# Kernel tuning notes

Measured on AMD Instinct MI355X. Metric: run time of the kernel, lower is better.

## Reference

```python
import jax, jax.numpy as jnp
import numpy as np

B, D_SENS, D_IDX, D_INT, D_OUT = 512, 784, 64, 32, 10
M = 262144  # eidetic memory entries


def setup_inputs() -> dict:
    key = jax.random.key(0)
    ks = jax.random.split(key, 12)
    s = lambda fan_in: 1.0 / np.sqrt(fan_in)
    return {
        "x_sensory": jax.random.normal(ks[0], (B, D_SENS), jnp.float32),
        "W1": jax.random.uniform(ks[1], (D_IDX, D_SENS), jnp.float32, -s(D_SENS), s(D_SENS)),
        "b1": jax.random.uniform(ks[2], (D_IDX,), jnp.float32, -s(D_SENS), s(D_SENS)),
        "W2": jax.random.uniform(ks[3], (D_INT, D_IDX), jnp.float32, -s(D_IDX), s(D_IDX)),
        "b2": jax.random.uniform(ks[4], (D_INT,), jnp.float32, -s(D_IDX), s(D_IDX)),
        "W3": jax.random.uniform(ks[5], (D_INT, D_SENS), jnp.float32, -s(D_SENS), s(D_SENS)),
        "b3": jax.random.uniform(ks[6], (D_INT,), jnp.float32, -s(D_SENS), s(D_SENS)),
        "W4": jax.random.uniform(ks[7], (D_OUT, D_INT), jnp.float32, -s(D_INT), s(D_INT)),
        "b4": jax.random.uniform(ks[8], (D_OUT,), jnp.float32, -s(D_INT), s(D_INT)),
        "mem_keys": jax.random.normal(ks[9], (M, D_IDX), jnp.float32),
        "mem_values": jax.random.normal(ks[10], (M, D_SENS), jnp.float32),
    }


def reference(x_sensory, W1, b1, W2, b2, W3, b3, W4, b4, mem_keys, mem_values):
    # indexer activations [B, 64]
    a_idx = jax.nn.relu(x_sensory @ W1.T + b1)
    # eidetic memory: nearest-neighbor lookup over stored indexer keys
    # squared L2 distances [B, M] via expansion (query norm is constant per row, omitted)
    d = jnp.sum(mem_keys * mem_keys, axis=1)[None, :] - 2.0 * (a_idx @ mem_keys.T)
    nn_idx = jnp.argmin(d, axis=1)  # [B]
    x_recaller = mem_values[nn_idx]  # [B, 784] irregular gather
    # integrator
    a_int = jax.nn.relu(a_idx @ W2.T + b2 + x_recaller @ W3.T + b3)
    return a_int @ W4.T + b4
```

## Files before the change

### kernel.cpp

```cpp
#include <hip/hip_runtime.h>
#include <stdint.h>

#define B_SZ   512
#define D_SENS 784
#define D_IDX  64
#define D_INT  32
#define D_OUT  10
#define M_ENT  262144
#define NCHUNK (M_ENT / 64)
#define MARGIN 1.5f

typedef __attribute__((ext_vector_type(8))) short bf16x8;
typedef __attribute__((ext_vector_type(4))) float f32x4;

__device__ inline unsigned short f2bf_rne(float f) {
    unsigned int u = __float_as_uint(f);
    unsigned int r = u + 0x7fffu + ((u >> 16) & 1u);
    return (unsigned short)(r >> 16);
}
__device__ inline unsigned int pack2bf_t(float lo, float hi) {
    return (__float_as_uint(lo) >> 16) | (__float_as_uint(hi) & 0xFFFF0000u);
}

__global__ __launch_bounds__(256) void k_front(const float* __restrict__ x,
                                               const float* __restrict__ W1,
                                               const float* __restrict__ b1,
                                               float* __restrict__ a_out,
                                               unsigned short* __restrict__ a_bf,
                                               unsigned long long* __restrict__ best) {
    int b = blockIdx.x, tid = threadIdx.x;
    __shared__ float xs[D_SENS];
    if (tid < 196) ((float4*)xs)[tid] = ((const float4*)(x + (size_t)b * D_SENS))[tid];
    if (tid == 0) best[b] = ~0ULL;
    __syncthreads();
    int i = tid >> 2, sub = tid & 3;
    const float4* wr = (const float4*)(W1 + (size_t)i * D_SENS);
    const float4* xs4 = (const float4*)xs;
    float a0 = 0.f, a1 = 0.f, a2 = 0.f, a3 = 0.f;
    #pragma unroll 7
    for (int jj = 0; jj < 49; ++jj) {
        float4 w = wr[sub + 4 * jj];
        float4 xv = xs4[sub + 4 * jj];
        a0 += w.x * xv.x; a1 += w.y * xv.y; a2 += w.z * xv.z; a3 += w.w * xv.w;
    }
    float s = (a0 + a1) + (a2 + a3);
    s += __shfl_xor(s, 1, 64);
    s += __shfl_xor(s, 2, 64);
    if (sub == 0) {
        float v = s + b1[i];
        float r = v > 0.f ? v : 0.f;
        a_out[b * D_IDX + i] = r;
        a_bf[b * D_IDX + i] = f2bf_rne(r);
    }
}

__global__ __launch_bounds__(256) void k_screen(const float* __restrict__ keys,
                                                const unsigned short* __restrict__ ab,
                                                float* __restrict__ chunkmin) {
    __shared__ unsigned short qlds[B_SZ * D_IDX];
    __shared__ float cms[8][B_SZ];
    int tid = threadIdx.x;
    int lane = tid & 63, wid = tid >> 6;
    int l15 = lane & 15, lg = lane >> 4;

    {
        int r = tid >> 3, j = tid & 7;
        #pragma unroll
        for (int pass = 0; pass < 16; ++pass, r += 32) {
            uint4 v = *(const uint4*)((const char*)ab + r * 128 + j * 16);
            int boff = r * 128 + ((j * 16) ^ ((r & 7) << 4));
            *(uint4*)((char*)qlds + boff) = v;
        }
    }

    int mbase = blockIdx.x * 512 + wid * 128;
    bf16x8 kf[8][2];
    f32x4 nrmv[8];
    #pragma unroll
    for (int t = 0; t < 8; ++t) {
        const float* rowp = keys + (size_t)(mbase + 16 * t + l15) * D_IDX;
        float4 f0 = *(const float4*)(rowp + lg * 8);
        float4 f1 = *(const float4*)(rowp + lg * 8 + 4);
        float4 f2 = *(const float4*)(rowp + 32 + lg * 8);
        float4 f3 = *(const float4*)(rowp + 32 + lg * 8 + 4);
        uint4 kp0, kp1;
        kp0.x = pack2bf_t(f0.x, f0.y); kp0.y = pack2bf_t(f0.z, f0.w);
        kp0.z = pack2bf_t(f1.x, f1.y); kp0.w = pack2bf_t(f1.z, f1.w);
        kp1.x = pack2bf_t(f2.x, f2.y); kp1.y = pack2bf_t(f2.z, f2.w);
        kp1.z = pack2bf_t(f3.x, f3.y); kp1.w = pack2bf_t(f3.z, f3.w);
        kf[t][0] = __builtin_bit_cast(bf16x8, kp0);
        kf[t][1] = __builtin_bit_cast(bf16x8, kp1);
        float s = f0.x*f0.x + f0.y*f0.y + f0.z*f0.z + f0.w*f0.w
                + f1.x*f1.x + f1.y*f1.y + f1.z*f1.z + f1.w*f1.w
                + f2.x*f2.x + f2.y*f2.y + f2.z*f2.z + f2.w*f2.w
                + f3.x*f3.x + f3.y*f3.y + f3.z*f3.z + f3.w*f3.w;
        s += __shfl_xor(s, 16, 64);
        s += __shfl_xor(s, 32, 64);
        s *= -0.5f;
        float n0 = __shfl(s, lg * 4 + 0, 64);
        float n1 = __shfl(s, lg * 4 + 1, 64);
        float n2 = __shfl(s, lg * 4 + 2, 64);
        float n3 = __shfl(s, lg * 4 + 3, 64);
        nrmv[t] = (f32x4){n0, n1, n2, n3};
    }
    __syncthreads();

    int colbase0 = lg * 16;
    int colbase1 = 64 + lg * 16;
    int rsw = (l15 & 7) << 4;
    int r0 = l15 * 128 + (colbase0 ^ rsw);
    int r1 = l15 * 128 + (colbase1 ^ rsw);
    bf16x8 q0 = *(const bf16x8*)((const char*)qlds + r0);
    bf16x8 q1 = *(const bf16x8*)((const char*)qlds + r1);

    for (int qt = 0; qt < 32; ++qt) {
        bf16x8 c0 = q0, c1 = q1;
        if (qt < 31) {
            q0 = *(const bf16x8*)((const char*)qlds + r0 + (qt + 1) * 2048);
            q1 = *(const bf16x8*)((const char*)qlds + r1 + (qt + 1) * 2048);
        }
        f32x4 acc[8];
        #pragma unroll
        for (int t = 0; t < 8; ++t)
            acc[t] = __builtin_amdgcn_mfma_f32_16x16x32_bf16(kf[t][0], c0, nrmv[t], 0, 0, 0);
        #pragma unroll
        for (int t = 0; t < 8; ++t)
            acc[t] = __builtin_amdgcn_mfma_f32_16x16x32_bf16(kf[t][1], c1, acc[t], 0, 0, 0);

        #pragma unroll
        for (int h = 0; h < 2; ++h) {
            int tb = h * 4;
            float t0 = fmaxf(fmaxf(acc[tb+0][0], acc[tb+0][1]), acc[tb+0][2]);
            float t1 = fmaxf(fmaxf(acc[tb+0][3], acc[tb+1][0]), acc[tb+1][1]);
            float t2 = fmaxf(fmaxf(acc[tb+1][2], acc[tb+1][3]), acc[tb+2][0]);
            float t3 = fmaxf(fmaxf(acc[tb+2][1], acc[tb+2][2]), acc[tb+2][3]);
            float t4 = fmaxf(fmaxf(acc[tb+3][0], acc[tb+3][1]), acc[tb+3][2]);
            float mx = fmaxf(fmaxf(fmaxf(t0, t1), fmaxf(t2, t3)), fmaxf(t4, acc[tb+3][3]));
            mx = fmaxf(mx, __shfl_xor(mx, 16, 64));
            mx = fmaxf(mx, __shfl_xor(mx, 32, 64));
            if (lane < 16) cms[wid * 2 + h][qt * 16 + lane] = -2.0f * mx;
        }
    }
    #pragma unroll
    for (int h = 0; h < 2; ++h) {
        int row = wid * 2 + h;
        float4 s0 = *(const float4*)&cms[row][lane * 8];
        float4 s1 = *(const float4*)&cms[row][lane * 8 + 4];
        float4* dst = (float4*)(chunkmin + (size_t)(blockIdx.x * 8 + row) * B_SZ + lane * 8);
        dst[0] = s0; dst[1] = s1;
    }
}

__global__ __launch_bounds__(256) void k_back(const float* __restrict__ chunkmin,
                                              const float* __restrict__ keys,
                                              const float* __restrict__ a_idx,
                                              const unsigned long long* __restrict__ bestg,
                                              const float* __restrict__ mem_values,
                                              const float* __restrict__ W2,
                                              const float* __restrict__ b2,
                                              const float* __restrict__ W3,
                                              const float* __restrict__ b3,
                                              const float* __restrict__ W4,
                                              const float* __restrict__ b4,
                                              float* __restrict__ out) {
    int q = blockIdx.x, tid = threadIdx.x;
    int lane = tid & 63;
    __shared__ float a_s[D_IDX];
    __shared__ float red[256];
    __shared__ int list[256];
    __shared__ int cnt;
    __shared__ unsigned long long bestsh;
    __shared__ float xr[D_SENS];
    __shared__ float ai[D_INT];

    if (tid < 16) ((float4*)a_s)[tid] = ((const float4*)(a_idx + q * D_IDX))[tid];
    if (tid == 0) { cnt = 0; bestsh = ~0ULL; }
    __syncthreads();

    if (chunkmin != nullptr) {
        float v[16];
        float lm = INFINITY;
        #pragma unroll
        for (int i = 0; i < 16; ++i) {
            v[i] = chunkmin[(size_t)(tid + 256 * i) * B_SZ + q];
            lm = fminf(lm, v[i]);
        }
        red[tid] = lm;
        __syncthreads();
        for (int s = 128; s > 0; s >>= 1) {
            if (tid < s) red[tid] = fminf(red[tid], red[tid + s]);
            __syncthreads();
        }
        float thrv = red[0] + MARGIN;
        #pragma unroll
        for (int i = 0; i < 16; ++i)
            if (v[i] <= thrv) { int p = atomicAdd(&cnt, 1); if (p < 256) list[p] = tid + 256 * i; }
        __syncthreads();
        int n = cnt > 256 ? 256 : cnt;

        unsigned long long bestp = ~0ULL;
        int kq = tid >> 2, qtr = tid & 3;
        for (int e = 0; e < n; ++e) {
            int m = list[e] * 64 + kq;
            const float4* kp = (const float4*)(keys + (size_t)m * D_IDX + qtr * 16);
            const float4* av = (const float4*)(a_s + qtr * 16);
            float p = 0.f, p2 = 0.f;
            #pragma unroll
            for (int j = 0; j < 4; ++j) {
                float4 kv = kp[j], av4 = av[j];
                p  += kv.x * av4.x + kv.y * av4.y + kv.z * av4.z + kv.w * av4.w;
                p2 += kv.x * kv.x + kv.y * kv.y + kv.z * kv.z + kv.w * kv.w;
            }
            p  += __shfl_xor(p, 1, 64);  p  += __shfl_xor(p, 2, 64);
            p2 += __shfl_xor(p2, 1, 64); p2 += __shfl_xor(p2, 2, 64);
            if (qtr == 0) {
                float d = p2 - 2.0f * p;
                unsigned int db = __float_as_uint(d);
                unsigned int ok = (db & 0x80000000u) ? ~db : (db | 0x80000000u);
                unsigned long long packed = ((unsigned long long)ok << 32) | (unsigned int)m;
                bestp = packed < bestp ? packed : bestp;
            }
        }
        #pragma unroll
        for (int off = 32; off >= 1; off >>= 1) {
            unsigned long long o = __shfl_xor(bestp, off, 64);
            bestp = o < bestp ? o : bestp;
        }
        if (lane == 0) atomicMin(&bestsh, bestp);
        __syncthreads();
    } else {
        if (tid == 0) bestsh = bestg[q];
        __syncthreads();
    }

    unsigned int idx = (unsigned int)(bestsh & 0xFFFFFFFFull);
    if (tid < 196) ((float4*)xr)[tid] = ((const float4*)(mem_values + (size_t)idx * D_SENS))[tid];
    __syncthreads();

    int i = tid >> 3, sub = tid & 7;
    const float* w3r = W3 + (size_t)i * D_SENS;
    float a0 = 0.f, a1 = 0.f, a2 = 0.f, a3 = 0.f;
    #pragma unroll 6
    for (int jj = 0; jj < 24; ++jj) {
        float4 w = *(const float4*)(w3r + sub * 4 + 32 * jj);
        float4 xv = *(const float4*)(xr + sub * 4 + 32 * jj);
        a0 += w.x * xv.x; a1 += w.y * xv.y; a2 += w.z * xv.z; a3 += w.w * xv.w;
    }
    if (sub < 4) {
        float4 w = *(const float4*)(w3r + 768 + sub * 4);
        float4 xv = *(const float4*)(xr + 768 + sub * 4);
        a0 += w.x * xv.x; a1 += w.y * xv.y; a2 += w.z * xv.z; a3 += w.w * xv.w;
    }
    const float* w2r = W2 + (size_t)i * D_IDX;
    #pragma unroll
    for (int jj = 0; jj < 2; ++jj) {
        float4 w = *(const float4*)(w2r + sub * 4 + 32 * jj);
        float4 av = *(const float4*)(a_s + sub * 4 + 32 * jj);
        a0 += w.x * av.x; a1 += w.y * av.y; a2 += w.z * av.z; a3 += w.w * av.w;
    }
    float s = (a0 + a1) + (a2 + a3);
    s += __shfl_xor(s, 1, 64);
    s += __shfl_xor(s, 2, 64);
    s += __shfl_xor(s, 4, 64);
    if (sub == 0) {
        float acc = s + b2[i] + b3[i];
        ai[i] = acc > 0.f ? acc : 0.f;
    }
    __syncthreads();
    if (tid < D_OUT) {
        float acc = b4[tid];
        const float* w4 = W4 + tid * D_INT;
        #pragma unroll
        for (int j = 0; j < D_INT; ++j) acc += w4[j] * ai[j];
        out[q * D_OUT + tid] = acc;
    }
}

__global__ void k_norms(const float* __restrict__ keys, float* __restrict__ norms) {
    int m = blockIdx.x * 256 + threadIdx.x;
    const float4* kp = (const float4*)(keys + (size_t)m * D_IDX);
    float a0 = 0.f, a1 = 0.f, a2 = 0.f, a3 = 0.f;
    #pragma unroll
    for (int t = 0; t < 16; t += 4) {
        float4 v0 = kp[t], v1 = kp[t + 1], v2 = kp[t + 2], v3 = kp[t + 3];
        a0 += v0.x * v0.x + v0.y * v0.y + v0.z * v0.z + v0.w * v0.w;
        a1 += v1.x * v1.x + v1.y * v1.y + v1.z * v1.z + v1.w * v1.w;
        a2 += v2.x * v2.x + v2.y * v2.y + v2.z * v2.z + v2.w * v2.w;
        a3 += v3.x * v3.x + v3.y * v3.y + v3.z * v3.z + v3.w * v3.w;
    }
    norms[m] = (a0 + a1) + (a2 + a3);
}

__global__ __launch_bounds__(256) void k_argmin(const float* __restrict__ keys,
                                                const float* __restrict__ norms,
                                                const float* __restrict__ a_idx,
                                                unsigned long long* __restrict__ best) {
    int q = blockIdx.y * 256 + threadIdx.x;
    float a[D_IDX];
    const float4* ap = (const float4*)(a_idx + (size_t)q * D_IDX);
    #pragma unroll
    for (int t = 0; t < 16; ++t) {
        float4 v = ap[t];
        a[4*t+0] = v.x; a[4*t+1] = v.y; a[4*t+2] = v.z; a[4*t+3] = v.w;
    }
    int m0 = blockIdx.x * 512;
    float bestd = INFINITY;
    int besti = 0;
    for (int i = 0; i < 512; ++i) {
        int m = m0 + i;
        const float* kp = keys + (size_t)m * D_IDX;
        float d0 = 0.f, d1 = 0.f, d2 = 0.f, d3 = 0.f;
        #pragma unroll
        for (int j = 0; j < D_IDX; j += 4) {
            d0 += kp[j+0] * a[j+0];
            d1 += kp[j+1] * a[j+1];
            d2 += kp[j+2] * a[j+2];
            d3 += kp[j+3] * a[j+3];
        }
        float dot = (d0 + d1) + (d2 + d3);
        float d = norms[m] - 2.0f * dot;
        if (d < bestd) { bestd = d; besti = m; }
    }
    unsigned int db = __float_as_uint(bestd);
    unsigned int okey = (db & 0x80000000u) ? ~db : (db | 0x80000000u);
    atomicMin(best + q, ((unsigned long long)okey << 32) | (unsigned int)besti);
}

extern "C" void kernel_launch(void* const* d_in, const int* in_sizes, int n_in,
                              void* d_out, int out_size, void* d_ws, size_t ws_size,
                              hipStream_t stream) {
    const float* x_sensory  = (const float*)d_in[0];
    const float* W1         = (const float*)d_in[1];
    const float* b1         = (const float*)d_in[2];
    const float* W2         = (const float*)d_in[3];
    const float* b2         = (const float*)d_in[4];
    const float* W3         = (const float*)d_in[5];
    const float* b3         = (const float*)d_in[6];
    const float* W4         = (const float*)d_in[7];
    const float* b4         = (const float*)d_in[8];
    const float* mem_keys   = (const float*)d_in[9];
    const float* mem_values = (const float*)d_in[10];
    float* out = (float*)d_out;

    char* ws = (char*)d_ws;
    unsigned long long* best = (unsigned long long*)ws;
    float*          a_idx    = (float*)(ws + 4096);
    unsigned short* a_bf     = (unsigned short*)(ws + 135168);
    float*          chunkmin = (float*)(ws + 200704);
    const size_t NEEDED = 200704 + (size_t)NCHUNK * B_SZ * 4;

    if (ws_size >= NEEDED) {
        k_front<<<B_SZ, 256, 0, stream>>>(x_sensory, W1, b1, a_idx, a_bf, best);
        k_screen<<<M_ENT / 512, 256, 0, stream>>>(mem_keys, a_bf, chunkmin);
        k_back<<<B_SZ, 256, 0, stream>>>(chunkmin, mem_keys, a_idx, nullptr, mem_values,
                                         W2, b2, W3, b3, W4, b4, out);
    } else {
        float* norms = (float*)(ws + 200704);
        k_front<<<B_SZ, 256, 0, stream>>>(x_sensory, W1, b1, a_idx, a_bf, best);
        k_norms<<<M_ENT / 256, 256, 0, stream>>>(mem_keys, norms);
        k_argmin<<<dim3(M_ENT / 512, 2), 256, 0, stream>>>(mem_keys, norms, a_idx, best);
        k_back<<<B_SZ, 256, 0, stream>>>(nullptr, mem_keys, a_idx, best, mem_values,
                                         W2, b2, W3, b3, W4, b4, out);
    }
}
```

Baseline: 62.42 us.

## Fuse front, screen and back kernels into one persistent kernel with grid barriers

Merges the three launches into a single kernel of 256 blocks that run each phase in turn and separate them with software grid-wide barriers built on atomic counters. Each block now handles two queries in the front and back phases and two 512-key tiles in the screening phase. This removes launch gaps and inter-kernel drains, at the cost of half as many blocks for the screen phase, 80KB of static LDS per block, and a memset launch. The barrier deadlocks unless all 256 blocks are resident at once.

Result: slower. 133.4 us (+113.7%).

```diff
diff --git a/kernel.cpp b/kernel.cpp
--- a/kernel.cpp
+++ b/kernel.cpp
@@ -9,6 +9,7 @@
 #define M_ENT  262144
 #define NCHUNK (M_ENT / 64)
 #define MARGIN 1.5f
+#define GRID_F 256
 
 typedef __attribute__((ext_vector_type(8))) short bf16x8;
 typedef __attribute__((ext_vector_type(4))) float f32x4;
@@ -20,6 +21,277 @@
 }
 __device__ inline unsigned int pack2bf_t(float lo, float hi) {
     return (__float_as_uint(lo) >> 16) | (__float_as_uint(hi) & 0xFFFF0000u);
+}
+
+__device__ inline void grid_bar(unsigned int* cnt) {
+    __syncthreads();
+    if (threadIdx.x == 0) {
+        __threadfence();
+        unsigned int old = atomicAdd(cnt, 1u);
+        unsigned int target = old - (old % GRID_F) + GRID_F;
+        while (__hip_atomic_load(cnt, __ATOMIC_RELAXED, __HIP_MEMORY_SCOPE_AGENT) < target)
+            __builtin_amdgcn_s_sleep(2);
+        __threadfence();
+    }
+    __syncthreads();
+}
+
+struct BackS {
+    float a_s[D_IDX];
+    float red[256];
+    int   list[256];
+    int   cnt;
+    unsigned long long bestsh;
+    float xr[D_SENS];
+    float ai[D_INT];
+};
+
+__global__ __launch_bounds__(256) void k_fused(
+    const float* __restrict__ x, const float* __restrict__ W1, const float* __restrict__ b1,
+    const float* __restrict__ W2, const float* __restrict__ b2,
+    const float* __restrict__ W3, const float* __restrict__ b3,
+    const float* __restrict__ W4, const float* __restrict__ b4,
+    const float* __restrict__ keys, const float* __restrict__ mem_values,
+    float* __restrict__ a_idx, unsigned short* __restrict__ a_bf,
+    float* __restrict__ chunkmin, unsigned int* __restrict__ bar,
+    float* __restrict__ out)
+{
+    __shared__ __align__(16) char smem[81920];
+    int bid = blockIdx.x, tid = threadIdx.x;
+    int lane = tid & 63, wid = tid >> 6;
+
+    {
+        float* xs = (float*)smem;
+        #pragma unroll 1
+        for (int bb = 0; bb < 2; ++bb) {
+            int b = bid * 2 + bb;
+            if (tid < 196) ((float4*)xs)[tid] = ((const float4*)(x + (size_t)b * D_SENS))[tid];
+            __syncthreads();
+            int i = tid >> 2, sub = tid & 3;
+            const float4* wr = (const float4*)(W1 + (size_t)i * D_SENS);
+            const float4* xs4 = (const float4*)xs;
+            float a0 = 0.f, a1 = 0.f, a2 = 0.f, a3 = 0.f;
+            #pragma unroll 7
+            for (int jj = 0; jj < 49; ++jj) {
+                float4 w = wr[sub + 4 * jj];
+                float4 xv = xs4[sub + 4 * jj];
+                a0 += w.x * xv.x; a1 += w.y * xv.y; a2 += w.z * xv.z; a3 += w.w * xv.w;
+            }
+            float s = (a0 + a1) + (a2 + a3);
+            s += __shfl_xor(s, 1, 64);
+            s += __shfl_xor(s, 2, 64);
+            if (sub == 0) {
+                float v = s + b1[i];
+                float r = v > 0.f ? v : 0.f;
+                a_idx[b * D_IDX + i] = r;
+                a_bf[b * D_IDX + i] = f2bf_rne(r);
+            }
+            __syncthreads();
+        }
+    }
+    grid_bar(bar + 0);
+
+    {
+        unsigned short* qlds = (unsigned short*)smem;
+        float (*cms)[B_SZ] = (float(*)[B_SZ])(smem + 65536);
+        int l15 = lane & 15, lg = lane >> 4;
+
+        {
+            int r = tid >> 3, j = tid & 7;
+            #pragma unroll
+            for (int pass = 0; pass < 16; ++pass, r += 32) {
+                uint4 v = *(const uint4*)((const char*)a_bf + r * 128 + j * 16);
+                int boff = r * 128 + ((j * 16) ^ ((r & 7) << 4));
+                *(uint4*)((char*)qlds + boff) = v;
+            }
+        }
+        __syncthreads();
+
+        int rsw = (l15 & 7) << 4;
+        int r0 = l15 * 128 + ((lg * 16) ^ rsw);
+        int r1 = l15 * 128 + ((64 + lg * 16) ^ rsw);
+
+        #pragma unroll 1
+        for (int p = 0; p < 2; ++p) {
+            int mbase = bid * 1024 + p * 512 + wid * 128;
+            bf16x8 kf[8][2];
+            f32x4 nrmv[8];
+            #pragma unroll
+            for (int t = 0; t < 8; ++t) {
+                const float* rowp = keys + (size_t)(mbase + 16 * t + l15) * D_IDX;
+                float4 f0 = *(const float4*)(rowp + lg * 8);
+                float4 f1 = *(const float4*)(rowp + lg * 8 + 4);
+                float4 f2 = *(const float4*)(rowp + 32 + lg * 8);
+                float4 f3 = *(const float4*)(rowp + 32 + lg * 8 + 4);
+                uint4 kp0, kp1;
+                kp0.x = pack2bf_t(f0.x, f0.y); kp0.y = pack2bf_t(f0.z, f0.w);
+                kp0.z = pack2bf_t(f1.x, f1.y); kp0.w = pack2bf_t(f1.z, f1.w);
+                kp1.x = pack2bf_t(f2.x, f2.y); kp1.y = pack2bf_t(f2.z, f2.w);
+                kp1.z = pack2bf_t(f3.x, f3.y); kp1.w = pack2bf_t(f3.z, f3.w);
+                kf[t][0] = __builtin_bit_cast(bf16x8, kp0);
+                kf[t][1] = __builtin_bit_cast(bf16x8, kp1);
+                float s = f0.x*f0.x + f0.y*f0.y + f0.z*f0.z + f0.w*f0.w
+                        + f1.x*f1.x + f1.y*f1.y + f1.z*f1.z + f1.w*f1.w
+                        + f2.x*f2.x + f2.y*f2.y + f2.z*f2.z + f2.w*f2.w
+                        + f3.x*f3.x + f3.y*f3.y + f3.z*f3.z + f3.w*f3.w;
+                s += __shfl_xor(s, 16, 64);
+                s += __shfl_xor(s, 32, 64);
+                s *= -0.5f;
+                float n0 = __shfl(s, lg * 4 + 0, 64);
+                float n1 = __shfl(s, lg * 4 + 1, 64);
+                float n2 = __shfl(s, lg * 4 + 2, 64);
+                float n3 = __shfl(s, lg * 4 + 3, 64);
+                nrmv[t] = (f32x4){n0, n1, n2, n3};
+            }
+
+            bf16x8 q0 = *(const bf16x8*)((const char*)qlds + r0);
+            bf16x8 q1 = *(const bf16x8*)((const char*)qlds + r1);
+
+            for (int qt = 0; qt < 32; ++qt) {
+                bf16x8 c0 = q0, c1 = q1;
+                if (qt < 31) {
+                    q0 = *(const bf16x8*)((const char*)qlds + r0 + (qt + 1) * 2048);
+                    q1 = *(const bf16x8*)((const char*)qlds + r1 + (qt + 1) * 2048);
+                }
+                f32x4 acc[8];
+                #pragma unroll
+                for (int t = 0; t < 8; ++t)
+                    acc[t] = __builtin_amdgcn_mfma_f32_16x16x32_bf16(kf[t][0], c0, nrmv[t], 0, 0, 0);
+                #pragma unroll
+                for (int t = 0; t < 8; ++t)
+                    acc[t] = __builtin_amdgcn_mfma_f32_16x16x32_bf16(kf[t][1], c1, acc[t], 0, 0, 0);
+
+                #pragma unroll
+                for (int h = 0; h < 2; ++h) {
+                    int tb = h * 4;
+                    float t0 = fmaxf(fmaxf(acc[tb+0][0], acc[tb+0][1]), acc[tb+0][2]);
+                    float t1 = fmaxf(fmaxf(acc[tb+0][3], acc[tb+1][0]), acc[tb+1][1]);
+                    float t2 = fmaxf(fmaxf(acc[tb+1][2], acc[tb+1][3]), acc[tb+2][0]);
+                    float t3 = fmaxf(fmaxf(acc[tb+2][1], acc[tb+2][2]), acc[tb+2][3]);
+                    float t4 = fmaxf(fmaxf(acc[tb+3][0], acc[tb+3][1]), acc[tb+3][2]);
+                    float mx = fmaxf(fmaxf(fmaxf(t0, t1), fmaxf(t2, t3)), fmaxf(t4, acc[tb+3][3]));
+                    mx = fmaxf(mx, __shfl_xor(mx, 16, 64));
+                    mx = fmaxf(mx, __shfl_xor(mx, 32, 64));
+                    if (lane < 16) cms[wid * 2 + h][qt * 16 + lane] = -2.0f * mx;
+                }
+            }
+            #pragma unroll
+            for (int h = 0; h < 2; ++h) {
+                int row = wid * 2 + h;
+                float4 s0 = *(const float4*)&cms[row][lane * 8];
+                float4 s1 = *(const float4*)&cms[row][lane * 8 + 4];
+                float4* dst = (float4*)(chunkmin + (size_t)(bid * 16 + p * 8 + row) * B_SZ + lane * 8);
+                dst[0] = s0; dst[1] = s1;
+            }
+            __syncthreads();
+        }
+    }
+    grid_bar(bar + 32);
+
+    {
+        BackS* bs = (BackS*)smem;
+        #pragma unroll 1
+        for (int qq = 0; qq < 2; ++qq) {
+            int q = bid * 2 + qq;
+            if (tid < 16) ((float4*)bs->a_s)[tid] = ((const float4*)(a_idx + q * D_IDX))[tid];
+            if (tid == 0) { bs->cnt = 0; bs->bestsh = ~0ULL; }
+            __syncthreads();
+
+            float v[16];
+            float lm = INFINITY;
+            #pragma unroll
+            for (int i2 = 0; i2 < 16; ++i2) {
+                v[i2] = chunkmin[(size_t)(tid + 256 * i2) * B_SZ + q];
+                lm = fminf(lm, v[i2]);
+            }
+            bs->red[tid] = lm;
+            __syncthreads();
+            for (int s2 = 128; s2 > 0; s2 >>= 1) {
+                if (tid < s2) bs->red[tid] = fminf(bs->red[tid], bs->red[tid + s2]);
+                __syncthreads();
+            }
+            float thrv = bs->red[0] + MARGIN;
+            #pragma unroll
+            for (int i2 = 0; i2 < 16; ++i2)
+                if (v[i2] <= thrv) { int p2 = atomicAdd(&bs->cnt, 1); if (p2 < 256) bs->list[p2] = tid + 256 * i2; }
+            __syncthreads();
+            int n = bs->cnt > 256 ? 256 : bs->cnt;
+
+            unsigned long long bestp = ~0ULL;
+            int kq = tid >> 2, qtr = tid & 3;
+            for (int e = 0; e < n; ++e) {
+                int m = bs->list[e] * 64 + kq;
+                const float4* kp = (const float4*)(keys + (size_t)m * D_IDX + qtr * 16);
+                const float4* av = (const float4*)(bs->a_s + qtr * 16);
+                float p = 0.f, p2 = 0.f;
+                #pragma unroll
+                for (int j = 0; j < 4; ++j) {
+                    float4 kv = kp[j], a4 = av[j];
+                    p  += kv.x * a4.x + kv.y * a4.y + kv.z * a4.z + kv.w * a4.w;
+                    p2 += kv.x * kv.x + kv.y * kv.y + kv.z * kv.z + kv.w * kv.w;
+                }
+                p  += __shfl_xor(p, 1, 64);  p  += __shfl_xor(p, 2, 64);
+                p2 += __shfl_xor(p2, 1, 64); p2 += __shfl_xor(p2, 2, 64);
+                if (qtr == 0) {
+                    float d = p2 - 2.0f * p;
+                    unsigned int db = __float_as_uint(d);
+                    unsigned int ok = (db & 0x80000000u) ? ~db : (db | 0x80000000u);
+                    unsigned long long packed = ((unsigned long long)ok << 32) | (unsigned int)m;
+                    bestp = packed < bestp ? packed : bestp;
+                }
+            }
+            #pragma unroll
+            for (int off = 32; off >= 1; off >>= 1) {
+                unsigned long long o = __shfl_xor(bestp, off, 64);
+                bestp = o < bestp ? o : bestp;
+            }
+            if (lane == 0) atomicMin(&bs->bestsh, bestp);
+            __syncthreads();
+
+            unsigned int idx = (unsigned int)(bs->bestsh & 0xFFFFFFFFull);
+            if (tid < 196) ((float4*)bs->xr)[tid] = ((const float4*)(mem_values + (size_t)idx * D_SENS))[tid];
+            __syncthreads();
+
+            int i = tid >> 3, sub = tid & 7;
+            const float* w3r = W3 + (size_t)i * D_SENS;
+            float a0 = 0.f, a1 = 0.f, a2 = 0.f, a3 = 0.f;
+            #pragma unroll 6
+            for (int jj = 0; jj < 24; ++jj) {
+                float4 w = *(const float4*)(w3r + sub * 4 + 32 * jj);
+                float4 xv = *(const float4*)(bs->xr + sub * 4 + 32 * jj);
+                a0 += w.x * xv.x; a1 += w.y * xv.y; a2 += w.z * xv.z; a3 += w.w * xv.w;
+            }
+            if (sub < 4) {
+                float4 w = *(const float4*)(w3r + 768 + sub * 4);
+                float4 xv = *(const float4*)(bs->xr + 768 + sub * 4);
+                a0 += w.x * xv.x; a1 += w.y * xv.y; a2 += w.z * xv.z; a3 += w.w * xv.w;
+            }
+            const float* w2r = W2 + (size_t)i * D_IDX;
+            #pragma unroll
+            for (int jj = 0; jj < 2; ++jj) {
+                float4 w = *(const float4*)(w2r + sub * 4 + 32 * jj);
+                float4 av = *(const float4*)(bs->a_s + sub * 4 + 32 * jj);
+                a0 += w.x * av.x; a1 += w.y * av.y; a2 += w.z * av.z; a3 += w.w * av.w;
+            }
+            float s = (a0 + a1) + (a2 + a3);
+            s += __shfl_xor(s, 1, 64);
+            s += __shfl_xor(s, 2, 64);
+            s += __shfl_xor(s, 4, 64);
+            if (sub == 0) {
+                float acc = s + b2[i] + b3[i];
+                bs->ai[i] = acc > 0.f ? acc : 0.f;
+            }
+            __syncthreads();
+            if (tid < D_OUT) {
+                float acc = b4[tid];
+                const float* w4 = W4 + tid * D_INT;
+                #pragma unroll
+                for (int j = 0; j < D_INT; ++j) acc += w4[j] * bs->ai[j];
+                out[q * D_OUT + tid] = acc;
+            }
+            __syncthreads();
+        }
+    }
 }
 
 __global__ __launch_bounds__(256) void k_front(const float* __restrict__ x,
@@ -51,228 +323,6 @@
         float r = v > 0.f ? v : 0.f;
         a_out[b * D_IDX + i] = r;
         a_bf[b * D_IDX + i] = f2bf_rne(r);
-    }
-}
-
-__global__ __launch_bounds__(256) void k_screen(const float* __restrict__ keys,
-                                                const unsigned short* __restrict__ ab,
-                                                float* __restrict__ chunkmin) {
-    __shared__ unsigned short qlds[B_SZ * D_IDX];
-    __shared__ float cms[8][B_SZ];
-    int tid = threadIdx.x;
-    int lane = tid & 63, wid = tid >> 6;
-    int l15 = lane & 15, lg = lane >> 4;
-
-    {
-        int r = tid >> 3, j = tid & 7;
-        #pragma unroll
-        for (int pass = 0; pass < 16; ++pass, r += 32) {
-            uint4 v = *(const uint4*)((const char*)ab + r * 128 + j * 16);
-            int boff = r * 128 + ((j * 16) ^ ((r & 7) << 4));
-            *(uint4*)((char*)qlds + boff) = v;
-        }
-    }
-
-    int mbase = blockIdx.x * 512 + wid * 128;
-    bf16x8 kf[8][2];
-    f32x4 nrmv[8];
-    #pragma unroll
-    for (int t = 0; t < 8; ++t) {
-        const float* rowp = keys + (size_t)(mbase + 16 * t + l15) * D_IDX;
-        float4 f0 = *(const float4*)(rowp + lg * 8);
-        float4 f1 = *(const float4*)(rowp + lg * 8 + 4);
-        float4 f2 = *(const float4*)(rowp + 32 + lg * 8);
-        float4 f3 = *(const float4*)(rowp + 32 + lg * 8 + 4);
-        uint4 kp0, kp1;
-        kp0.x = pack2bf_t(f0.x, f0.y); kp0.y = pack2bf_t(f0.z, f0.w);
-        kp0.z = pack2bf_t(f1.x, f1.y); kp0.w = pack2bf_t(f1.z, f1.w);
-        kp1.x = pack2bf_t(f2.x, f2.y); kp1.y = pack2bf_t(f2.z, f2.w);
-        kp1.z = pack2bf_t(f3.x, f3.y); kp1.w = pack2bf_t(f3.z, f3.w);
-        kf[t][0] = __builtin_bit_cast(bf16x8, kp0);
-        kf[t][1] = __builtin_bit_cast(bf16x8, kp1);
-        float s = f0.x*f0.x + f0.y*f0.y + f0.z*f0.z + f0.w*f0.w
-                + f1.x*f1.x + f1.y*f1.y + f1.z*f1.z + f1.w*f1.w
-                + f2.x*f2.x + f2.y*f2.y + f2.z*f2.z + f2.w*f2.w
-                + f3.x*f3.x + f3.y*f3.y + f3.z*f3.z + f3.w*f3.w;
-        s += __shfl_xor(s, 16, 64);
-        s += __shfl_xor(s, 32, 64);
-        s *= -0.5f;
-        float n0 = __shfl(s, lg * 4 + 0, 64);
-        float n1 = __shfl(s, lg * 4 + 1, 64);
-        float n2 = __shfl(s, lg * 4 + 2, 64);
-        float n3 = __shfl(s, lg * 4 + 3, 64);
-        nrmv[t] = (f32x4){n0, n1, n2, n3};
-    }
-    __syncthreads();
-
-    int colbase0 = lg * 16;
-    int colbase1 = 64 + lg * 16;
-    int rsw = (l15 & 7) << 4;
-    int r0 = l15 * 128 + (colbase0 ^ rsw);
-    int r1 = l15 * 128 + (colbase1 ^ rsw);
-    bf16x8 q0 = *(const bf16x8*)((const char*)qlds + r0);
-    bf16x8 q1 = *(const bf16x8*)((const char*)qlds + r1);
-
-    for (int qt = 0; qt < 32; ++qt) {
-        bf16x8 c0 = q0, c1 = q1;
-        if (qt < 31) {
-            q0 = *(const bf16x8*)((const char*)qlds + r0 + (qt + 1) * 2048);
-            q1 = *(const bf16x8*)((const char*)qlds + r1 + (qt + 1) * 2048);
-        }
-        f32x4 acc[8];
-        #pragma unroll
-        for (int t = 0; t < 8; ++t)
-            acc[t] = __builtin_amdgcn_mfma_f32_16x16x32_bf16(kf[t][0], c0, nrmv[t], 0, 0, 0);
-        #pragma unroll
-        for (int t = 0; t < 8; ++t)
-            acc[t] = __builtin_amdgcn_mfma_f32_16x16x32_bf16(kf[t][1], c1, acc[t], 0, 0, 0);
-
-        #pragma unroll
-        for (int h = 0; h < 2; ++h) {
-            int tb = h * 4;
-            float t0 = fmaxf(fmaxf(acc[tb+0][0], acc[tb+0][1]), acc[tb+0][2]);
-            float t1 = fmaxf(fmaxf(acc[tb+0][3], acc[tb+1][0]), acc[tb+1][1]);
-            float t2 = fmaxf(fmaxf(acc[tb+1][2], acc[tb+1][3]), acc[tb+2][0]);
-            float t3 = fmaxf(fmaxf(acc[tb+2][1], acc[tb+2][2]), acc[tb+2][3]);
-            float t4 = fmaxf(fmaxf(acc[tb+3][0], acc[tb+3][1]), acc[tb+3][2]);
-            float mx = fmaxf(fmaxf(fmaxf(t0, t1), fmaxf(t2, t3)), fmaxf(t4, acc[tb+3][3]));
-            mx = fmaxf(mx, __shfl_xor(mx, 16, 64));
-            mx = fmaxf(mx, __shfl_xor(mx, 32, 64));
-            if (lane < 16) cms[wid * 2 + h][qt * 16 + lane] = -2.0f * mx;
-        }
-    }
-    #pragma unroll
-    for (int h = 0; h < 2; ++h) {
-        int row = wid * 2 + h;
-        float4 s0 = *(const float4*)&cms[row][lane * 8];
-        float4 s1 = *(const float4*)&cms[row][lane * 8 + 4];
-        float4* dst = (float4*)(chunkmin + (size_t)(blockIdx.x * 8 + row) * B_SZ + lane * 8);
-        dst[0] = s0; dst[1] = s1;
-    }
-}
-
-__global__ __launch_bounds__(256) void k_back(const float* __restrict__ chunkmin,
-                                              const float* __restrict__ keys,
-                                              const float* __restrict__ a_idx,
-                                              const unsigned long long* __restrict__ bestg,
-                                              const float* __restrict__ mem_values,
-                                              const float* __restrict__ W2,
-                                              const float* __restrict__ b2,
-                                              const float* __restrict__ W3,
-                                              const float* __restrict__ b3,
-                                              const float* __restrict__ W4,
-                                              const float* __restrict__ b4,
-                                              float* __restrict__ out) {
-    int q = blockIdx.x, tid = threadIdx.x;
-    int lane = tid & 63;
-    __shared__ float a_s[D_IDX];
-    __shared__ float red[256];
-    __shared__ int list[256];
-    __shared__ int cnt;
-    __shared__ unsigned long long bestsh;
-    __shared__ float xr[D_SENS];
-    __shared__ float ai[D_INT];
-
-    if (tid < 16) ((float4*)a_s)[tid] = ((const float4*)(a_idx + q * D_IDX))[tid];
-    if (tid == 0) { cnt = 0; bestsh = ~0ULL; }
-    __syncthreads();
-
-    if (chunkmin != nullptr) {
-        float v[16];
-        float lm = INFINITY;
-        #pragma unroll
-        for (int i = 0; i < 16; ++i) {
-            v[i] = chunkmin[(size_t)(tid + 256 * i) * B_SZ + q];
-            lm = fminf(lm, v[i]);
-        }
-        red[tid] = lm;
-        __syncthreads();
-        for (int s = 128; s > 0; s >>= 1) {
-            if (tid < s) red[tid] = fminf(red[tid], red[tid + s]);
-            __syncthreads();
-        }
-        float thrv = red[0] + MARGIN;
-        #pragma unroll
-        for (int i = 0; i < 16; ++i)
-            if (v[i] <= thrv) { int p = atomicAdd(&cnt, 1); if (p < 256) list[p] = tid + 256 * i; }
-        __syncthreads();
-        int n = cnt > 256 ? 256 : cnt;
-
-        unsigned long long bestp = ~0ULL;
-        int kq = tid >> 2, qtr = tid & 3;
-        for (int e = 0; e < n; ++e) {
-            int m = list[e] * 64 + kq;
-            const float4* kp = (const float4*)(keys + (size_t)m * D_IDX + qtr * 16);
-            const float4* av = (const float4*)(a_s + qtr * 16);
-            float p = 0.f, p2 = 0.f;
-            #pragma unroll
-            for (int j = 0; j < 4; ++j) {
-                float4 kv = kp[j], av4 = av[j];
-                p  += kv.x * av4.x + kv.y * av4.y + kv.z * av4.z + kv.w * av4.w;
-                p2 += kv.x * kv.x + kv.y * kv.y + kv.z * kv.z + kv.w * kv.w;
-            }
-            p  += __shfl_xor(p, 1, 64);  p  += __shfl_xor(p, 2, 64);
-            p2 += __shfl_xor(p2, 1, 64); p2 += __shfl_xor(p2, 2, 64);
-            if (qtr == 0) {
-                float d = p2 - 2.0f * p;
-                unsigned int db = __float_as_uint(d);
-                unsigned int ok = (db & 0x80000000u) ? ~db : (db | 0x80000000u);
-                unsigned long long packed = ((unsigned long long)ok << 32) | (unsigned int)m;
-                bestp = packed < bestp ? packed : bestp;
-            }
-        }
-        #pragma unroll
-        for (int off = 32; off >= 1; off >>= 1) {
-            unsigned long long o = __shfl_xor(bestp, off, 64);
-            bestp = o < bestp ? o : bestp;
-        }
-        if (lane == 0) atomicMin(&bestsh, bestp);
-        __syncthreads();
-    } else {
-        if (tid == 0) bestsh = bestg[q];
-        __syncthreads();
-    }
-
-    unsigned int idx = (unsigned int)(bestsh & 0xFFFFFFFFull);
-    if (tid < 196) ((float4*)xr)[tid] = ((const float4*)(mem_values + (size_t)idx * D_SENS))[tid];
-    __syncthreads();
-
-    int i = tid >> 3, sub = tid & 7;
-    const float* w3r = W3 + (size_t)i * D_SENS;
-    float a0 = 0.f, a1 = 0.f, a2 = 0.f, a3 = 0.f;
-    #pragma unroll 6
-    for (int jj = 0; jj < 24; ++jj) {
-        float4 w = *(const float4*)(w3r + sub * 4 + 32 * jj);
-        float4 xv = *(const float4*)(xr + sub * 4 + 32 * jj);
-        a0 += w.x * xv.x; a1 += w.y * xv.y; a2 += w.z * xv.z; a3 += w.w * xv.w;
-    }
-    if (sub < 4) {
-        float4 w = *(const float4*)(w3r + 768 + sub * 4);
-        float4 xv = *(const float4*)(xr + 768 + sub * 4);
-        a0 += w.x * xv.x; a1 += w.y * xv.y; a2 += w.z * xv.z; a3 += w.w * xv.w;
-    }
-    const float* w2r = W2 + (size_t)i * D_IDX;
-    #pragma unroll
-    for (int jj = 0; jj < 2; ++jj) {
-        float4 w = *(const float4*)(w2r + sub * 4 + 32 * jj);
-        float4 av = *(const float4*)(a_s + sub * 4 + 32 * jj);
-        a0 += w.x * av.x; a1 += w.y * av.y; a2 += w.z * av.z; a3 += w.w * av.w;
-    }
-    float s = (a0 + a1) + (a2 + a3);
-    s += __shfl_xor(s, 1, 64);
-    s += __shfl_xor(s, 2, 64);
-    s += __shfl_xor(s, 4, 64);
-    if (sub == 0) {
-        float acc = s + b2[i] + b3[i];
-        ai[i] = acc > 0.f ? acc : 0.f;
-    }
-    __syncthreads();
-    if (tid < D_OUT) {
-        float acc = b4[tid];
-        const float* w4 = W4 + tid * D_INT;
-        #pragma unroll
-        for (int j = 0; j < D_INT; ++j) acc += w4[j] * ai[j];
-        out[q * D_OUT + tid] = acc;
     }
 }
 
@@ -326,6 +376,65 @@
     atomicMin(best + q, ((unsigned long long)okey << 32) | (unsigned int)besti);
 }
 
+__global__ __launch_bounds__(256) void k_back_fb(const float* __restrict__ keys,
+                                                 const float* __restrict__ a_idx,
+                                                 const unsigned long long* __restrict__ bestg,
+                                                 const float* __restrict__ mem_values,
+                                                 const float* __restrict__ W2,
+                                                 const float* __restrict__ b2,
+                                                 const float* __restrict__ W3,
+                                                 const float* __restrict__ b3,
+                                                 const float* __restrict__ W4,
+                                                 const float* __restrict__ b4,
+                                                 float* __restrict__ out) {
+    int q = blockIdx.x, tid = threadIdx.x;
+    __shared__ float a_s[D_IDX];
+    __shared__ float xr[D_SENS];
+    __shared__ float ai[D_INT];
+    if (tid < 16) ((float4*)a_s)[tid] = ((const float4*)(a_idx + q * D_IDX))[tid];
+    __syncthreads();
+    unsigned int idx = (unsigned int)(bestg[q] & 0xFFFFFFFFull);
+    if (tid < 196) ((float4*)xr)[tid] = ((const float4*)(mem_values + (size_t)idx * D_SENS))[tid];
+    __syncthreads();
+    int i = tid >> 3, sub = tid & 7;
+    const float* w3r = W3 + (size_t)i * D_SENS;
+    float a0 = 0.f, a1 = 0.f, a2 = 0.f, a3 = 0.f;
+    #pragma unroll 6
+    for (int jj = 0; jj < 24; ++jj) {
+        float4 w = *(const float4*)(w3r + sub * 4 + 32 * jj);
+        float4 xv = *(const float4*)(xr + sub * 4 + 32 * jj);
+        a0 += w.x * xv.x; a1 += w.y * xv.y; a2 += w.z * xv.z; a3 += w.w * xv.w;
+    }
+    if (sub < 4) {
+        float4 w = *(const float4*)(w3r + 768 + sub * 4);
+        float4 xv = *(const float4*)(xr + 768 + sub * 4);
+        a0 += w.x * xv.x; a1 += w.y * xv.y; a2 += w.z * xv.z; a3 += w.w * xv.w;
+    }
+    const float* w2r = W2 + (size_t)i * D_IDX;
+    #pragma unroll
+    for (int jj = 0; jj < 2; ++jj) {
+        float4 w = *(const float4*)(w2r + sub * 4 + 32 * jj);
+        float4 av = *(const float4*)(a_s + sub * 4 + 32 * jj);
+        a0 += w.x * av.x; a1 += w.y * av.y; a2 += w.z * av.z; a3 += w.w * av.w;
+    }
+    float s = (a0 + a1) + (a2 + a3);
+    s += __shfl_xor(s, 1, 64);
+    s += __shfl_xor(s, 2, 64);
+    s += __shfl_xor(s, 4, 64);
+    if (sub == 0) {
+        float acc = s + b2[i] + b3[i];
+        ai[i] = acc > 0.f ? acc : 0.f;
+    }
+    __syncthreads();
+    if (tid < D_OUT) {
+        float acc = b4[tid];
+        const float* w4 = W4 + tid * D_INT;
+        #pragma unroll
+        for (int j = 0; j < D_INT; ++j) acc += w4[j] * ai[j];
+        out[q * D_OUT + tid] = acc;
+    }
+}
+
 extern "C" void kernel_launch(void* const* d_in, const int* in_sizes, int n_in,
                               void* d_out, int out_size, void* d_ws, size_t ws_size,
                               hipStream_t stream) {
@@ -343,23 +452,24 @@
     float* out = (float*)d_out;
 
     char* ws = (char*)d_ws;
-    unsigned long long* best = (unsigned long long*)ws;
-    float*          a_idx    = (float*)(ws + 4096);
-    unsigned short* a_bf     = (unsigned short*)(ws + 135168);
-    float*          chunkmin = (float*)(ws + 200704);
-    const size_t NEEDED = 200704 + (size_t)NCHUNK * B_SZ * 4;
+    unsigned int*       bar      = (unsigned int*)ws;
+    unsigned long long* best     = (unsigned long long*)(ws + 4096);
+    float*              a_idx    = (float*)(ws + 8192);
+    unsigned short*     a_bf     = (unsigned short*)(ws + 139264);
+    float*              chunkmin = (float*)(ws + 204800);
+    const size_t NEEDED = 204800 + (size_t)NCHUNK * B_SZ * 4;
 
     if (ws_size >= NEEDED) {
-        k_front<<<B_SZ, 256, 0, stream>>>(x_sensory, W1, b1, a_idx, a_bf, best);
-        k_screen<<<M_ENT / 512, 256, 0, stream>>>(mem_keys, a_bf, chunkmin);
-        k_back<<<B_SZ, 256, 0, stream>>>(chunkmin, mem_keys, a_idx, nullptr, mem_values,
-                                         W2, b2, W3, b3, W4, b4, out);
+        hipMemsetAsync(bar, 0, 256, stream);
+        k_fused<<<GRID_F, 256, 0, stream>>>(x_sensory, W1, b1, W2, b2, W3, b3, W4, b4,
+                                            mem_keys, mem_values, a_idx, a_bf,
+                                            chunkmin, bar, out);
     } else {
-        float* norms = (float*)(ws + 200704);
+        float* norms = chunkmin;
         k_front<<<B_SZ, 256, 0, stream>>>(x_sensory, W1, b1, a_idx, a_bf, best);
         k_norms<<<M_ENT / 256, 256, 0, stream>>>(mem_keys, norms);
         k_argmin<<<dim3(M_ENT / 512, 2), 256, 0, stream>>>(mem_keys, norms, a_idx, best);
-        k_back<<<B_SZ, 256, 0, stream>>>(nullptr, mem_keys, a_idx, best, mem_values,
-                                         W2, b2, W3, b3, W4, b4, out);
-    }
-}
+        k_back_fb<<<B_SZ, 256, 0, stream>>>(mem_keys, a_idx, best, mem_values,
+                                            W2, b2, W3, b3, W4, b4, out);
+    }
+}
```
